# Kernel optimization log

Hardware: AMD Instinct MI355X
Metric: run time of the kernel (lower is better)

## Reference

```python
import jax, jax.numpy as jnp
import numpy as np

N_NODES = 50000
N_EDGES = 800000
IN_C, HID_C, OUT_C = 128, 128, 64


def setup_inputs() -> dict:
    key = jax.random.key(0)
    ks = jax.random.split(key, 12)
    glorot = lambda k, shape: jax.random.normal(k, shape, dtype=jnp.float32) * (2.0 / (shape[0] + shape[-1])) ** 0.5
    return {
        "x": jax.random.normal(ks[0], (N_NODES, IN_C), dtype=jnp.float32),
        "edge_index": jax.random.randint(ks[1], (2, N_EDGES), 0, N_NODES, dtype=jnp.int64),
        "W_s1": glorot(ks[2], (IN_C, HID_C)), "b_s1": jnp.zeros((HID_C,), jnp.float32),
        "W_s2": glorot(ks[3], (HID_C, HID_C)), "b_s2": jnp.zeros((HID_C,), jnp.float32),
        "W_m1": glorot(ks[4], (IN_C, HID_C)), "b_m1": jnp.zeros((HID_C,), jnp.float32),
        "W_m21": glorot(ks[5], (IN_C, HID_C)), "b_m21": jnp.zeros((HID_C,), jnp.float32),
        "W_m22": glorot(ks[6], (HID_C, HID_C)), "b_m22": jnp.zeros((HID_C,), jnp.float32),
        "W_att": glorot(ks[7], (HID_C, 1)), "b_att": jnp.zeros((1,), jnp.float32),
        "W_fc": glorot(ks[8], (2 * HID_C, OUT_C)), "b_fc": jnp.zeros((OUT_C,), jnp.float32),
    }


def _gcn_conv(x, W, b, src, dst, n_nodes):
    """PyG GCNConv: add self-loops, symmetric deg^-1/2 norm, linear, scatter-add, bias."""
    xw = x @ W  # [N, H]
    loop = jnp.arange(n_nodes, dtype=src.dtype)
    s = jnp.concatenate([src, loop])
    d = jnp.concatenate([dst, loop])
    ones = jnp.ones(s.shape[0], dtype=x.dtype)
    deg = jax.ops.segment_sum(ones, d, num_segments=n_nodes)  # in-degree incl. self loop
    dinv = jnp.where(deg > 0, jax.lax.rsqrt(deg), 0.0)
    norm = dinv[s] * dinv[d]  # [E+N]
    msg = xw[s] * norm[:, None]
    return jax.ops.segment_sum(msg, d, num_segments=n_nodes) + b


def reference(x, edge_index, W_s1, b_s1, W_s2, b_s2, W_m1, b_m1, W_m21, b_m21,
              W_m22, b_m22, W_att, b_att, W_fc, b_fc):
    n = x.shape[0]
    src, dst = edge_index[0], edge_index[1]
    # structural branch: two GCN layers
    h_struct = jax.nn.relu(_gcn_conv(x, W_s1, b_s1, src, dst, n))
    h_struct = jax.nn.relu(_gcn_conv(h_struct, W_s2, b_s2, src, dst, n))
    # meta branches
    h1 = jax.nn.relu(_gcn_conv(x, W_m1, b_m1, src, dst, n))
    h2 = jax.nn.relu(_gcn_conv(x, W_m21, b_m21, src, dst, n))
    h2 = jax.nn.relu(_gcn_conv(h2, W_m22, b_m22, src, dst, n))
    # attention-weighted fusion over the 2 branches
    H = jnp.stack([h1, h2], axis=1)  # [N, 2, H]
    attn_scores = H @ W_att + b_att  # [N, 2, 1]
    attn_weights = jax.nn.softmax(attn_scores, axis=1)
    h_meta = jnp.sum(attn_weights * H, axis=1)  # [N, H]
    h_comb = jnp.concatenate([h_struct, h_meta], axis=1)  # [N, 2H]
    return h_comb @ W_fc + b_fc  # [N, OUT_C]
```

## Files before the change

kernel.cpp:

```cpp
#include <hip/hip_runtime.h>
#include <hip/hip_bf16.h>

#define N_NODES 50000
#define N_EDGES 800000
#define IN_C 128
#define HID_C 128
#define OUT_C 64

#define SCAN_BS 256
#define SCAN_NB ((N_NODES + SCAN_BS - 1) / SCAN_BS)

#define PREP_CVT_NB   6250
#define PREP_DEG_NB   3125
#define PREP_WCAT_NB  192
#define PREP_TP_NB    64
#define PREP_NB (PREP_CVT_NB + PREP_DEG_NB + PREP_WCAT_NB + 3 * PREP_TP_NB)

typedef __attribute__((ext_vector_type(8))) short bf16x8;
typedef __attribute__((ext_vector_type(4))) float f32x4;

__device__ __forceinline__ ushort f2bf(float f) {
    unsigned u = __float_as_uint(f);
    return (ushort)((u + 0x7fffu + ((u >> 16) & 1u)) >> 16);
}
__device__ __forceinline__ float bf2f(ushort u) {
    return __uint_as_float(((unsigned)u) << 16);
}

__global__ __launch_bounds__(256)
void prep_kernel(const float* __restrict__ x, uint2* __restrict__ xb4,
                 const int* __restrict__ edst, int* __restrict__ hist,
                 const float* __restrict__ Ws1, const float* __restrict__ Wm21,
                 const float* __restrict__ Wm1,
                 const float* __restrict__ bs1, const float* __restrict__ bm21,
                 const float* __restrict__ bm1,
                 ushort* __restrict__ Wcat_t, float* __restrict__ bcat,
                 const float* __restrict__ Ws2, ushort* __restrict__ Ws2t,
                 const float* __restrict__ Wm22, ushort* __restrict__ Wm22t,
                 const float* __restrict__ Wfc, ushort* __restrict__ Wfct,
                 int* __restrict__ row_ptr) {
    const int bid = blockIdx.x;
    const int t = threadIdx.x;
    if (bid < PREP_CVT_NB) {
        int i = bid * 256 + t;
        float4 v = *(const float4*)&x[(size_t)i * 4];
        uint2 o;
        o.x = (uint)f2bf(v.x) | ((uint)f2bf(v.y) << 16);
        o.y = (uint)f2bf(v.z) | ((uint)f2bf(v.w) << 16);
        xb4[i] = o;
    } else if (bid < PREP_CVT_NB + PREP_DEG_NB) {
        int e = (bid - PREP_CVT_NB) * 256 + t;
        atomicAdd(&hist[edst[e]], 1);
    } else if (bid < PREP_CVT_NB + PREP_DEG_NB + PREP_WCAT_NB) {
        int idx = (bid - PREP_CVT_NB - PREP_DEG_NB) * 256 + t;
        int c = idx >> 7, k = idx & 127;
        float v = (c < 128) ? Ws1[k * 128 + c]
                : (c < 256) ? Wm21[k * 128 + (c - 128)]
                            : Wm1[k * 128 + (c - 256)];
        Wcat_t[idx] = f2bf(v);
        if (idx < 384) {
            bcat[idx] = (idx < 128) ? bs1[idx] : (idx < 256) ? bm21[idx - 128] : bm1[idx - 256];
        }
        if (idx == 0) row_ptr[N_NODES] = N_EDGES;
    } else if (bid < PREP_CVT_NB + PREP_DEG_NB + PREP_WCAT_NB + PREP_TP_NB) {
        int idx = (bid - PREP_CVT_NB - PREP_DEG_NB - PREP_WCAT_NB) * 256 + t;
        int c = idx >> 7, k = idx & 127;
        Ws2t[idx] = f2bf(Ws2[(size_t)k * 128 + c]);
    } else if (bid < PREP_CVT_NB + PREP_DEG_NB + PREP_WCAT_NB + 2 * PREP_TP_NB) {
        int idx = (bid - PREP_CVT_NB - PREP_DEG_NB - PREP_WCAT_NB - PREP_TP_NB) * 256 + t;
        int c = idx >> 7, k = idx & 127;
        Wm22t[idx] = f2bf(Wm22[(size_t)k * 128 + c]);
    } else {
        int idx = (bid - PREP_CVT_NB - PREP_DEG_NB - PREP_WCAT_NB - 2 * PREP_TP_NB) * 256 + t;
        int c = idx >> 8, k = idx & 255;
        Wfct[idx] = f2bf(Wfc[(size_t)k * 64 + c]);
    }
}

__global__ __launch_bounds__(SCAN_BS)
void scan1_kernel(const int* __restrict__ hist, int* __restrict__ bsum,
                  float* __restrict__ dinv, int n) {
    __shared__ int s[SCAN_BS];
    int t = threadIdx.x;
    int i = blockIdx.x * SCAN_BS + t;
    int v = (i < n) ? hist[i] : 0;
    if (i < n) dinv[i] = rsqrtf((float)(v + 1));
    s[t] = v;
    __syncthreads();
#pragma unroll
    for (int off = SCAN_BS / 2; off > 0; off >>= 1) {
        if (t < off) s[t] += s[t + off];
        __syncthreads();
    }
    if (t == 0) bsum[blockIdx.x] = s[0];
}

__global__ __launch_bounds__(SCAN_BS)
void scan3_kernel(const int* __restrict__ hist, const int* __restrict__ bsum,
                  int* __restrict__ row_ptr, int* __restrict__ cursor, int n) {
    __shared__ int s[SCAN_BS];
    __shared__ int pre_s;
    int t = threadIdx.x;
    int b = blockIdx.x;
    int p = 0;
    for (int j = t; j < b; j += SCAN_BS) p += bsum[j];
    s[t] = p;
    __syncthreads();
#pragma unroll
    for (int off = SCAN_BS / 2; off > 0; off >>= 1) {
        if (t < off) s[t] += s[t + off];
        __syncthreads();
    }
    if (t == 0) pre_s = s[0];
    __syncthreads();
    const int pre = pre_s;
    __syncthreads();
    int i = b * SCAN_BS + t;
    int v = (i < n) ? hist[i] : 0;
    s[t] = v;
    __syncthreads();
#pragma unroll
    for (int off = 1; off < SCAN_BS; off <<= 1) {
        int tmp = (t >= off) ? s[t - off] : 0;
        __syncthreads();
        s[t] += tmp;
        __syncthreads();
    }
    if (i < n) {
        int ex = s[t] - v + pre;
        row_ptr[i] = ex;
        cursor[i]  = ex;
    }
}

__global__ void fill_kernel(const int* __restrict__ src, const int* __restrict__ dst, int E,
                            int* __restrict__ cursor, int2* __restrict__ edge_data,
                            const float* __restrict__ dinv) {
    int e = blockIdx.x * blockDim.x + threadIdx.x;
    if (e < E) {
        int d = dst[e];
        int s = src[e];
        int pos = atomicAdd(&cursor[d], 1);
        edge_data[pos] = make_int2(s, __float_as_int(dinv[s]));
    }
}

template<int C>
__global__ __launch_bounds__(256)
void agg_bf16(const ushort* __restrict__ X, int ldx,
              ushort* __restrict__ Y, int ldy,
              const int* __restrict__ row_ptr,
              const int2* __restrict__ edge_data,
              const float* __restrict__ dinv, int n) {
    constexpr int CG = C / 8;
    constexpr int SLOTS = 64 / CG;
    const int wid = blockIdx.x * (blockDim.x >> 6) + (threadIdx.x >> 6);
    if (wid >= n) return;
    const int lane = threadIdx.x & 63;
    const int cg = lane & (CG - 1);
    const int slot = lane / CG;

    const float di = dinv[wid];
    float acc[8] = {0.f, 0.f, 0.f, 0.f, 0.f, 0.f, 0.f, 0.f};

    auto fma_row = [&](uint4 v, float w) {
        acc[0] = fmaf(w, __uint_as_float(v.x << 16), acc[0]);
        acc[1] = fmaf(w, __uint_as_float(v.x & 0xffff0000u), acc[1]);
        acc[2] = fmaf(w, __uint_as_float(v.y << 16), acc[2]);
        acc[3] = fmaf(w, __uint_as_float(v.y & 0xffff0000u), acc[3]);
        acc[4] = fmaf(w, __uint_as_float(v.z << 16), acc[4]);
        acc[5] = fmaf(w, __uint_as_float(v.z & 0xffff0000u), acc[5]);
        acc[6] = fmaf(w, __uint_as_float(v.w << 16), acc[6]);
        acc[7] = fmaf(w, __uint_as_float(v.w & 0xffff0000u), acc[7]);
    };

    if (slot == 0) {
        uint4 v = *(const uint4*)&X[(size_t)wid * ldx + cg * 8];
        fma_row(v, di * di);
    }
    const int e0 = row_ptr[wid], e1 = row_ptr[wid + 1];
    int e = e0 + slot;
    for (; e + 3 * SLOTS < e1; e += 4 * SLOTS) {
        const int2 d0 = edge_data[e];
        const int2 d1 = edge_data[e + SLOTS];
        const int2 d2 = edge_data[e + 2 * SLOTS];
        const int2 d3 = edge_data[e + 3 * SLOTS];
        const uint4 v0 = *(const uint4*)&X[(size_t)d0.x * ldx + cg * 8];
        const uint4 v1 = *(const uint4*)&X[(size_t)d1.x * ldx + cg * 8];
        const uint4 v2 = *(const uint4*)&X[(size_t)d2.x * ldx + cg * 8];
        const uint4 v3 = *(const uint4*)&X[(size_t)d3.x * ldx + cg * 8];
        fma_row(v0, di * __int_as_float(d0.y));
        fma_row(v1, di * __int_as_float(d1.y));
        fma_row(v2, di * __int_as_float(d2.y));
        fma_row(v3, di * __int_as_float(d3.y));
    }
    for (; e < e1; e += SLOTS) {
        const int2 d0 = edge_data[e];
        const uint4 v0 = *(const uint4*)&X[(size_t)d0.x * ldx + cg * 8];
        fma_row(v0, di * __int_as_float(d0.y));
    }
#pragma unroll
    for (int j = 0; j < 8; ++j) {
        if (SLOTS == 4) acc[j] += __shfl_xor(acc[j], 16);
        if (SLOTS >= 2) acc[j] += __shfl_xor(acc[j], 32);
    }
    if (slot == 0) {
        uint4 o;
        o.x = (uint)f2bf(acc[0]) | ((uint)f2bf(acc[1]) << 16);
        o.y = (uint)f2bf(acc[2]) | ((uint)f2bf(acc[3]) << 16);
        o.z = (uint)f2bf(acc[4]) | ((uint)f2bf(acc[5]) << 16);
        o.w = (uint)f2bf(acc[6]) | ((uint)f2bf(acc[7]) << 16);
        *(uint4*)&Y[(size_t)wid * ldy + cg * 8] = o;
    }
}

__global__ __launch_bounds__(256)
void mfma_gemm_kernel(const ushort* __restrict__ A, int lda,
                      const ushort* __restrict__ Wt,
                      const float* __restrict__ bias,
                      void* __restrict__ Yv, int ldy,
                      int M, int relu, int obf16) {
    __shared__ char Asmem[128 * 272];
    const int tid = threadIdx.x;
    const int lane = tid & 63;
    const int w = tid >> 6;
    const int rb = blockIdx.x * 128;
    const int cb = blockIdx.y * 128;

    {
        const int rowbase = tid >> 4;
        const int inrow = (tid & 15) * 8;
#pragma unroll
        for (int it = 0; it < 8; ++it) {
            int row = it * 16 + rowbase;
            uint4 v = make_uint4(0u, 0u, 0u, 0u);
            int r = rb + row;
            if (r < M) v = *(const uint4*)&A[(size_t)r * lda + inrow];
            *(uint4*)&Asmem[row * 272 + (tid & 15) * 16] = v;
        }
    }
    __syncthreads();

    f32x4 acc[2][8];
#pragma unroll
    for (int i = 0; i < 2; ++i)
#pragma unroll
        for (int j = 0; j < 8; ++j) acc[i][j] = (f32x4){0.f, 0.f, 0.f, 0.f};

    const int arow0 = w * 32 + (lane & 15);
    const int kq = (lane >> 4) * 8;
    const int ccol = lane & 15;
#pragma unroll
    for (int ks = 0; ks < 4; ++ks) {
        const int k0 = ks * 32;
        const bf16x8 a0 = *(const bf16x8*)&Asmem[arow0 * 272 + (k0 + kq) * 2];
        const bf16x8 a1 = *(const bf16x8*)&Asmem[(arow0 + 16) * 272 + (k0 + kq) * 2];
#pragma unroll
        for (int ct = 0; ct < 8; ++ct) {
            const bf16x8 b = *(const bf16x8*)&Wt[(size_t)(cb + ct * 16 + ccol) * 128 + k0 + kq];
            acc[0][ct] = __builtin_amdgcn_mfma_f32_16x16x32_bf16(a0, b, acc[0][ct], 0, 0, 0);
            acc[1][ct] = __builtin_amdgcn_mfma_f32_16x16x32_bf16(a1, b, acc[1][ct], 0, 0, 0);
        }
    }

    const int rowq = (lane >> 4) * 4;
#pragma unroll
    for (int rt = 0; rt < 2; ++rt) {
#pragma unroll
        for (int ct = 0; ct < 8; ++ct) {
            const int col = cb + ct * 16 + ccol;
            const float bcol = bias[col];
#pragma unroll
            for (int r = 0; r < 4; ++r) {
                const int row = rb + w * 32 + rt * 16 + rowq + r;
                if (row >= M) continue;
                float v = acc[rt][ct][r] + bcol;
                if (relu) v = fmaxf(v, 0.f);
                if (obf16) ((ushort*)Yv)[(size_t)row * ldy + col] = f2bf(v);
                else       ((float*)Yv)[(size_t)row * ldy + col] = v;
            }
        }
    }
}

__global__ __launch_bounds__(256)
void gemm2_kernel(const ushort* __restrict__ bufB,
                  const ushort* __restrict__ Ws2t, const float* __restrict__ bs2,
                  const ushort* __restrict__ Wm22t, const float* __restrict__ bm22,
                  const ushort* __restrict__ cat1,
                  const float* __restrict__ Watt, const float* __restrict__ batt,
                  ushort* __restrict__ comb, int M) {
    __shared__ char Asmem[128 * 272];
    const int tid = threadIdx.x;
    const int lane = tid & 63;
    const int w = tid >> 6;
    const int rb = blockIdx.x * 128;
    const int branch = blockIdx.y;
    const ushort* A = bufB + (branch ? 128 : 0);
    const ushort* Wt = branch ? Wm22t : Ws2t;
    const float* bias = branch ? bm22 : bs2;

    {
        const int rowbase = tid >> 4;
        const int seg = tid & 15;
#pragma unroll
        for (int it = 0; it < 8; ++it) {
            int row = it * 16 + rowbase;
            uint4 v = make_uint4(0u, 0u, 0u, 0u);
            int r = rb + row;
            if (r < M) v = *(const uint4*)&A[(size_t)r * 256 + seg * 8];
            *(uint4*)&Asmem[row * 272 + seg * 16] = v;
        }
    }
    __syncthreads();

    f32x4 acc[2][8];
#pragma unroll
    for (int i = 0; i < 2; ++i)
#pragma unroll
        for (int j = 0; j < 8; ++j) acc[i][j] = (f32x4){0.f, 0.f, 0.f, 0.f};

    const int arow0 = w * 32 + (lane & 15);
    const int kq = (lane >> 4) * 8;
    const int ccol = lane & 15;
#pragma unroll
    for (int ks = 0; ks < 4; ++ks) {
        const int k0 = ks * 32;
        const bf16x8 a0 = *(const bf16x8*)&Asmem[arow0 * 272 + (k0 + kq) * 2];
        const bf16x8 a1 = *(const bf16x8*)&Asmem[(arow0 + 16) * 272 + (k0 + kq) * 2];
#pragma unroll
        for (int ct = 0; ct < 8; ++ct) {
            const bf16x8 b = *(const bf16x8*)&Wt[(size_t)(ct * 16 + ccol) * 128 + k0 + kq];
            acc[0][ct] = __builtin_amdgcn_mfma_f32_16x16x32_bf16(a0, b, acc[0][ct], 0, 0, 0);
            acc[1][ct] = __builtin_amdgcn_mfma_f32_16x16x32_bf16(a1, b, acc[1][ct], 0, 0, 0);
        }
    }

    const int quad = lane >> 4;
    if (branch == 0) {
#pragma unroll
        for (int rt = 0; rt < 2; ++rt) {
#pragma unroll
            for (int ct = 0; ct < 8; ++ct) {
                const int col = ct * 16 + ccol;
                const float bcol = bias[col];
#pragma unroll
                for (int r = 0; r < 4; ++r) {
                    const int row = rb + w * 32 + rt * 16 + quad * 4 + r;
                    if (row >= M) continue;
                    comb[(size_t)row * 256 + col] = f2bf(fmaxf(acc[rt][ct][r] + bcol, 0.f));
                }
            }
        }
    } else {
#pragma unroll
        for (int rt = 0; rt < 2; ++rt)
#pragma unroll
            for (int ct = 0; ct < 8; ++ct) {
                const float bcol = bias[ct * 16 + ccol];
#pragma unroll
                for (int r = 0; r < 4; ++r)
                    acc[rt][ct][r] = fmaxf(acc[rt][ct][r] + bcol, 0.f);
            }
        float wv[8];
#pragma unroll
        for (int ct = 0; ct < 8; ++ct) wv[ct] = Watt[ct * 16 + ccol];
        const float ba = batt[0];
#pragma unroll
        for (int rt = 0; rt < 2; ++rt) {
#pragma unroll
            for (int r = 0; r < 4; ++r) {
                const int row0 = rb + w * 32 + rt * 16 + quad * 4 + r;
                const int rowc = (row0 < M) ? row0 : (M - 1);
                const ushort* h1row = &cat1[(size_t)rowc * 384 + 256];
                float bp = 0.f, ap = 0.f;
#pragma unroll
                for (int ct = 0; ct < 8; ++ct) {
                    bp += acc[rt][ct][r] * wv[ct];
                    ap += bf2f(h1row[ct * 16 + ccol]) * wv[ct];
                }
#pragma unroll
                for (int off = 1; off < 16; off <<= 1) {
                    bp += __shfl_xor(bp, off);
                    ap += __shfl_xor(ap, off);
                }
                const float a = ap + ba, b = bp + ba;
                const float m = fmaxf(a, b);
                const float ea = __expf(a - m), eb = __expf(b - m);
                const float inv = 1.f / (ea + eb);
                const float wa = ea * inv, wb = eb * inv;
                if (row0 < M) {
#pragma unroll
                    for (int ct = 0; ct < 8; ++ct) {
                        const float h1 = bf2f(h1row[ct * 16 + ccol]);
                        comb[(size_t)row0 * 256 + 128 + ct * 16 + ccol] =
                            f2bf(fmaf(wa, h1, wb * acc[rt][ct][r]));
                    }
                }
            }
        }
    }
}

__global__ __launch_bounds__(256)
void mfma_fc_kernel(const ushort* __restrict__ A,
                    const ushort* __restrict__ Wt,
                    const float* __restrict__ bias,
                    float* __restrict__ Y, int M) {
    __shared__ char Asmem[64 * 528];
    const int tid = threadIdx.x;
    const int lane = tid & 63;
    const int w = tid >> 6;
    const int rb = blockIdx.x * 64;

    {
        const int rowbase = tid >> 5;
        const int seg = (tid & 31);
#pragma unroll
        for (int it = 0; it < 8; ++it) {
            int row = it * 8 + rowbase;
            uint4 v = make_uint4(0u, 0u, 0u, 0u);
            int r = rb + row;
            if (r < M) v = *(const uint4*)&A[(size_t)r * 256 + seg * 8];
            *(uint4*)&Asmem[row * 528 + seg * 16] = v;
        }
    }
    __syncthreads();

    f32x4 acc[4];
#pragma unroll
    for (int j = 0; j < 4; ++j) acc[j] = (f32x4){0.f, 0.f, 0.f, 0.f};

    const int arow = w * 16 + (lane & 15);
    const int kq = (lane >> 4) * 8;
    const int ccol = lane & 15;
#pragma unroll
    for (int ks = 0; ks < 8; ++ks) {
        const int k0 = ks * 32;
        const bf16x8 a = *(const bf16x8*)&Asmem[arow * 528 + (k0 + kq) * 2];
#pragma unroll
        for (int ct = 0; ct < 4; ++ct) {
            const bf16x8 b = *(const bf16x8*)&Wt[(size_t)(ct * 16 + ccol) * 256 + k0 + kq];
            acc[ct] = __builtin_amdgcn_mfma_f32_16x16x32_bf16(a, b, acc[ct], 0, 0, 0);
        }
    }

    const int rowq = (lane >> 4) * 4;
#pragma unroll
    for (int ct = 0; ct < 4; ++ct) {
        const int col = ct * 16 + ccol;
        const float bcol = bias[col];
#pragma unroll
        for (int r = 0; r < 4; ++r) {
            const int row = rb + w * 16 + rowq + r;
            if (row < M) Y[(size_t)row * 64 + col] = acc[ct][r] + bcol;
        }
    }
}

extern "C" void kernel_launch(void* const* d_in, const int* in_sizes, int n_in,
                              void* d_out, int out_size, void* d_ws, size_t ws_size,
                              hipStream_t stream) {
    const int N = N_NODES, E = N_EDGES;
    const float* x     = (const float*)d_in[0];
    const int*   ei    = (const int*)d_in[1];
    const int*   esrc  = ei;
    const int*   edst  = ei + E;
    const float* W_s1  = (const float*)d_in[2];
    const float* b_s1  = (const float*)d_in[3];
    const float* W_s2  = (const float*)d_in[4];
    const float* b_s2  = (const float*)d_in[5];
    const float* W_m1  = (const float*)d_in[6];
    const float* b_m1  = (const float*)d_in[7];
    const float* W_m21 = (const float*)d_in[8];
    const float* b_m21 = (const float*)d_in[9];
    const float* W_m22 = (const float*)d_in[10];
    const float* b_m22 = (const float*)d_in[11];
    const float* W_att = (const float*)d_in[12];
    const float* b_att = (const float*)d_in[13];
    const float* W_fc  = (const float*)d_in[14];
    const float* b_fc  = (const float*)d_in[15];
    float* out = (float*)d_out;

    char* base = (char*)d_ws;
    size_t off = 0;
    auto take = [&](size_t nbytes) -> void* {
        void* p = base + off;
        off += (nbytes + 255) & ~(size_t)255;
        return p;
    };
    int*    hist      = (int*)take((size_t)N * 4);
    int*    cursor    = (int*)take((size_t)N * 4);
    int*    row_ptr   = (int*)take((size_t)(N + 1) * 4);
    int*    bsum      = (int*)take((size_t)SCAN_NB * 4);
    int2*   edge_data = (int2*)take((size_t)E * 8);
    float*  dinv      = (float*)take((size_t)N * 4);
    ushort* xb        = (ushort*)take((size_t)N * 128 * 2);
    ushort* agg_x     = (ushort*)take((size_t)N * 128 * 2);
    ushort* cat1      = (ushort*)take((size_t)N * 384 * 2);
    ushort* bufB      = (ushort*)take((size_t)N * 256 * 2);
    ushort* comb      = (ushort*)take((size_t)N * 256 * 2);
    ushort* Wcat_t    = (ushort*)take((size_t)384 * 128 * 2);
    ushort* Ws2_t     = (ushort*)take((size_t)128 * 128 * 2);
    ushort* Wm22_t    = (ushort*)take((size_t)128 * 128 * 2);
    ushort* Wfc_t     = (ushort*)take((size_t)64 * 256 * 2);
    float*  bcat      = (float*)take((size_t)384 * 4);

    hipMemsetAsync(hist, 0, (size_t)N * 4, stream);
    prep_kernel<<<PREP_NB, 256, 0, stream>>>(x, (uint2*)xb, edst, hist,
                                             W_s1, W_m21, W_m1, b_s1, b_m21, b_m1,
                                             Wcat_t, bcat, W_s2, Ws2_t, W_m22, Wm22_t,
                                             W_fc, Wfc_t, row_ptr);
    scan1_kernel<<<SCAN_NB, SCAN_BS, 0, stream>>>(hist, bsum, dinv, N);
    scan3_kernel<<<SCAN_NB, SCAN_BS, 0, stream>>>(hist, bsum, row_ptr, cursor, N);
    fill_kernel<<<(E + 255) / 256, 256, 0, stream>>>(esrc, edst, E, cursor, edge_data, dinv);

    agg_bf16<128><<<(N + 3) / 4, 256, 0, stream>>>(xb, 128, agg_x, 128, row_ptr, edge_data, dinv, N);
    dim3 gm384((N + 127) / 128, 3);
    mfma_gemm_kernel<<<gm384, 256, 0, stream>>>(agg_x, 128, Wcat_t, bcat, cat1, 384, N, 1, 1);
    agg_bf16<256><<<(N + 3) / 4, 256, 0, stream>>>(cat1, 384, bufB, 256, row_ptr, edge_data, dinv, N);
    dim3 gm2((N + 127) / 128, 2);
    gemm2_kernel<<<gm2, 256, 0, stream>>>(bufB, Ws2_t, b_s2, Wm22_t, b_m22,
                                          cat1, W_att, b_att, comb, N);
    mfma_fc_kernel<<<(N + 63) / 64, 256, 0, stream>>>(comb, Wfc_t, b_fc, out, N);
}
```

Baseline: 383.6 us.

## Fuse all pipeline stages into one persistent cooperative kernel with grid syncs

Replaces the sequence of separate kernels (prep, scans, CSR fill, two aggregations, three GEMMs) with a single cooperatively launched persistent kernel. Grid-wide barriers separate the stages and work is distributed with grid-stride loops. The aim is to remove per-launch overhead and the idle gaps between kernels. The cost is grid.sync overhead at each stage, occupancy capped by the largest stage's register and shared-memory needs, and less parallelism in the small stages.

```diff
diff --git a/kernel.cpp b/kernel.cpp
--- a/kernel.cpp
+++ b/kernel.cpp
@@ -1,20 +1,13 @@
 #include <hip/hip_runtime.h>
 #include <hip/hip_bf16.h>
+#include <hip/hip_cooperative_groups.h>
+
+namespace cg = cooperative_groups;
 
 #define N_NODES 50000
 #define N_EDGES 800000
-#define IN_C 128
-#define HID_C 128
-#define OUT_C 64
-
 #define SCAN_BS 256
 #define SCAN_NB ((N_NODES + SCAN_BS - 1) / SCAN_BS)
-
-#define PREP_CVT_NB   6250
-#define PREP_DEG_NB   3125
-#define PREP_WCAT_NB  192
-#define PREP_TP_NB    64
-#define PREP_NB (PREP_CVT_NB + PREP_DEG_NB + PREP_WCAT_NB + 3 * PREP_TP_NB)
 
 typedef __attribute__((ext_vector_type(8))) short bf16x8;
 typedef __attribute__((ext_vector_type(4))) float f32x4;
@@ -27,139 +20,31 @@
     return __uint_as_float(((unsigned)u) << 16);
 }
 
-__global__ __launch_bounds__(256)
-void prep_kernel(const float* __restrict__ x, uint2* __restrict__ xb4,
-                 const int* __restrict__ edst, int* __restrict__ hist,
-                 const float* __restrict__ Ws1, const float* __restrict__ Wm21,
-                 const float* __restrict__ Wm1,
-                 const float* __restrict__ bs1, const float* __restrict__ bm21,
-                 const float* __restrict__ bm1,
-                 ushort* __restrict__ Wcat_t, float* __restrict__ bcat,
-                 const float* __restrict__ Ws2, ushort* __restrict__ Ws2t,
-                 const float* __restrict__ Wm22, ushort* __restrict__ Wm22t,
-                 const float* __restrict__ Wfc, ushort* __restrict__ Wfct,
-                 int* __restrict__ row_ptr) {
-    const int bid = blockIdx.x;
-    const int t = threadIdx.x;
-    if (bid < PREP_CVT_NB) {
-        int i = bid * 256 + t;
-        float4 v = *(const float4*)&x[(size_t)i * 4];
-        uint2 o;
-        o.x = (uint)f2bf(v.x) | ((uint)f2bf(v.y) << 16);
-        o.y = (uint)f2bf(v.z) | ((uint)f2bf(v.w) << 16);
-        xb4[i] = o;
-    } else if (bid < PREP_CVT_NB + PREP_DEG_NB) {
-        int e = (bid - PREP_CVT_NB) * 256 + t;
-        atomicAdd(&hist[edst[e]], 1);
-    } else if (bid < PREP_CVT_NB + PREP_DEG_NB + PREP_WCAT_NB) {
-        int idx = (bid - PREP_CVT_NB - PREP_DEG_NB) * 256 + t;
-        int c = idx >> 7, k = idx & 127;
-        float v = (c < 128) ? Ws1[k * 128 + c]
-                : (c < 256) ? Wm21[k * 128 + (c - 128)]
-                            : Wm1[k * 128 + (c - 256)];
-        Wcat_t[idx] = f2bf(v);
-        if (idx < 384) {
-            bcat[idx] = (idx < 128) ? bs1[idx] : (idx < 256) ? bm21[idx - 128] : bm1[idx - 256];
-        }
-        if (idx == 0) row_ptr[N_NODES] = N_EDGES;
-    } else if (bid < PREP_CVT_NB + PREP_DEG_NB + PREP_WCAT_NB + PREP_TP_NB) {
-        int idx = (bid - PREP_CVT_NB - PREP_DEG_NB - PREP_WCAT_NB) * 256 + t;
-        int c = idx >> 7, k = idx & 127;
-        Ws2t[idx] = f2bf(Ws2[(size_t)k * 128 + c]);
-    } else if (bid < PREP_CVT_NB + PREP_DEG_NB + PREP_WCAT_NB + 2 * PREP_TP_NB) {
-        int idx = (bid - PREP_CVT_NB - PREP_DEG_NB - PREP_WCAT_NB - PREP_TP_NB) * 256 + t;
-        int c = idx >> 7, k = idx & 127;
-        Wm22t[idx] = f2bf(Wm22[(size_t)k * 128 + c]);
-    } else {
-        int idx = (bid - PREP_CVT_NB - PREP_DEG_NB - PREP_WCAT_NB - 2 * PREP_TP_NB) * 256 + t;
-        int c = idx >> 8, k = idx & 255;
-        Wfct[idx] = f2bf(Wfc[(size_t)k * 64 + c]);
-    }
-}
-
-__global__ __launch_bounds__(SCAN_BS)
-void scan1_kernel(const int* __restrict__ hist, int* __restrict__ bsum,
-                  float* __restrict__ dinv, int n) {
-    __shared__ int s[SCAN_BS];
-    int t = threadIdx.x;
-    int i = blockIdx.x * SCAN_BS + t;
-    int v = (i < n) ? hist[i] : 0;
-    if (i < n) dinv[i] = rsqrtf((float)(v + 1));
-    s[t] = v;
-    __syncthreads();
-#pragma unroll
-    for (int off = SCAN_BS / 2; off > 0; off >>= 1) {
-        if (t < off) s[t] += s[t + off];
-        __syncthreads();
-    }
-    if (t == 0) bsum[blockIdx.x] = s[0];
-}
-
-__global__ __launch_bounds__(SCAN_BS)
-void scan3_kernel(const int* __restrict__ hist, const int* __restrict__ bsum,
-                  int* __restrict__ row_ptr, int* __restrict__ cursor, int n) {
-    __shared__ int s[SCAN_BS];
-    __shared__ int pre_s;
-    int t = threadIdx.x;
-    int b = blockIdx.x;
-    int p = 0;
-    for (int j = t; j < b; j += SCAN_BS) p += bsum[j];
-    s[t] = p;
-    __syncthreads();
-#pragma unroll
-    for (int off = SCAN_BS / 2; off > 0; off >>= 1) {
-        if (t < off) s[t] += s[t + off];
-        __syncthreads();
-    }
-    if (t == 0) pre_s = s[0];
-    __syncthreads();
-    const int pre = pre_s;
-    __syncthreads();
-    int i = b * SCAN_BS + t;
-    int v = (i < n) ? hist[i] : 0;
-    s[t] = v;
-    __syncthreads();
-#pragma unroll
-    for (int off = 1; off < SCAN_BS; off <<= 1) {
-        int tmp = (t >= off) ? s[t - off] : 0;
-        __syncthreads();
-        s[t] += tmp;
-        __syncthreads();
-    }
-    if (i < n) {
-        int ex = s[t] - v + pre;
-        row_ptr[i] = ex;
-        cursor[i]  = ex;
-    }
-}
-
-__global__ void fill_kernel(const int* __restrict__ src, const int* __restrict__ dst, int E,
-                            int* __restrict__ cursor, int2* __restrict__ edge_data,
-                            const float* __restrict__ dinv) {
-    int e = blockIdx.x * blockDim.x + threadIdx.x;
-    if (e < E) {
-        int d = dst[e];
-        int s = src[e];
-        int pos = atomicAdd(&cursor[d], 1);
-        edge_data[pos] = make_int2(s, __float_as_int(dinv[s]));
-    }
-}
+struct MegaParams {
+    const float* x;
+    const int* esrc;
+    const int* edst;
+    const float *Ws1, *bs1, *Ws2, *bs2, *Wm1, *bm1, *Wm21, *bm21, *Wm22, *bm22;
+    const float *Watt, *batt, *Wfc, *bfc;
+    float* out;
+    int* hist; int* cursor; int* row_ptr; int* bsum;
+    int2* edge_data; float* dinv;
+    ushort *xb, *agg_x, *cat1, *bufB, *comb;
+    ushort *Wcat_t, *Ws2t, *Wm22t, *Wfct;
+    float* bcat;
+};
 
 template<int C>
-__global__ __launch_bounds__(256)
-void agg_bf16(const ushort* __restrict__ X, int ldx,
-              ushort* __restrict__ Y, int ldy,
-              const int* __restrict__ row_ptr,
-              const int2* __restrict__ edge_data,
-              const float* __restrict__ dinv, int n) {
+__device__ __forceinline__ void agg_node(const ushort* __restrict__ X, int ldx,
+                                         ushort* __restrict__ Y, int ldy,
+                                         const int* __restrict__ row_ptr,
+                                         const int2* __restrict__ edge_data,
+                                         const float* __restrict__ dinv,
+                                         int wid, int lane) {
     constexpr int CG = C / 8;
     constexpr int SLOTS = 64 / CG;
-    const int wid = blockIdx.x * (blockDim.x >> 6) + (threadIdx.x >> 6);
-    if (wid >= n) return;
-    const int lane = threadIdx.x & 63;
-    const int cg = lane & (CG - 1);
+    const int cgi = lane & (CG - 1);
     const int slot = lane / CG;
-
     const float di = dinv[wid];
     float acc[8] = {0.f, 0.f, 0.f, 0.f, 0.f, 0.f, 0.f, 0.f};
 
@@ -175,7 +60,7 @@
     };
 
     if (slot == 0) {
-        uint4 v = *(const uint4*)&X[(size_t)wid * ldx + cg * 8];
+        uint4 v = *(const uint4*)&X[(size_t)wid * ldx + cgi * 8];
         fma_row(v, di * di);
     }
     const int e0 = row_ptr[wid], e1 = row_ptr[wid + 1];
@@ -185,10 +70,10 @@
         const int2 d1 = edge_data[e + SLOTS];
         const int2 d2 = edge_data[e + 2 * SLOTS];
         const int2 d3 = edge_data[e + 3 * SLOTS];
-        const uint4 v0 = *(const uint4*)&X[(size_t)d0.x * ldx + cg * 8];
-        const uint4 v1 = *(const uint4*)&X[(size_t)d1.x * ldx + cg * 8];
-        const uint4 v2 = *(const uint4*)&X[(size_t)d2.x * ldx + cg * 8];
-        const uint4 v3 = *(const uint4*)&X[(size_t)d3.x * ldx + cg * 8];
+        const uint4 v0 = *(const uint4*)&X[(size_t)d0.x * ldx + cgi * 8];
+        const uint4 v1 = *(const uint4*)&X[(size_t)d1.x * ldx + cgi * 8];
+        const uint4 v2 = *(const uint4*)&X[(size_t)d2.x * ldx + cgi * 8];
+        const uint4 v3 = *(const uint4*)&X[(size_t)d3.x * ldx + cgi * 8];
         fma_row(v0, di * __int_as_float(d0.y));
         fma_row(v1, di * __int_as_float(d1.y));
         fma_row(v2, di * __int_as_float(d2.y));
@@ -196,7 +81,7 @@
     }
     for (; e < e1; e += SLOTS) {
         const int2 d0 = edge_data[e];
-        const uint4 v0 = *(const uint4*)&X[(size_t)d0.x * ldx + cg * 8];
+        const uint4 v0 = *(const uint4*)&X[(size_t)d0.x * ldx + cgi * 8];
         fma_row(v0, di * __int_as_float(d0.y));
     }
 #pragma unroll
@@ -210,33 +95,26 @@
         o.y = (uint)f2bf(acc[2]) | ((uint)f2bf(acc[3]) << 16);
         o.z = (uint)f2bf(acc[4]) | ((uint)f2bf(acc[5]) << 16);
         o.w = (uint)f2bf(acc[6]) | ((uint)f2bf(acc[7]) << 16);
-        *(uint4*)&Y[(size_t)wid * ldy + cg * 8] = o;
-    }
-}
-
-__global__ __launch_bounds__(256)
-void mfma_gemm_kernel(const ushort* __restrict__ A, int lda,
-                      const ushort* __restrict__ Wt,
-                      const float* __restrict__ bias,
-                      void* __restrict__ Yv, int ldy,
-                      int M, int relu, int obf16) {
-    __shared__ char Asmem[128 * 272];
-    const int tid = threadIdx.x;
+        *(uint4*)&Y[(size_t)wid * ldy + cgi * 8] = o;
+    }
+}
+
+__device__ __forceinline__ void gemm128_tile(char* smem,
+        const ushort* __restrict__ A, int lda,
+        const ushort* __restrict__ Wt, const float* __restrict__ bias,
+        ushort* __restrict__ Y, int ldy, int rb, int cb, int M, int tid) {
     const int lane = tid & 63;
     const int w = tid >> 6;
-    const int rb = blockIdx.x * 128;
-    const int cb = blockIdx.y * 128;
-
     {
         const int rowbase = tid >> 4;
-        const int inrow = (tid & 15) * 8;
+        const int seg = tid & 15;
 #pragma unroll
         for (int it = 0; it < 8; ++it) {
             int row = it * 16 + rowbase;
             uint4 v = make_uint4(0u, 0u, 0u, 0u);
             int r = rb + row;
-            if (r < M) v = *(const uint4*)&A[(size_t)r * lda + inrow];
-            *(uint4*)&Asmem[row * 272 + (tid & 15) * 16] = v;
+            if (r < M) v = *(const uint4*)&A[(size_t)r * lda + seg * 8];
+            *(uint4*)&smem[row * 272 + seg * 16] = v;
         }
     }
     __syncthreads();
@@ -253,8 +131,8 @@
 #pragma unroll
     for (int ks = 0; ks < 4; ++ks) {
         const int k0 = ks * 32;
-        const bf16x8 a0 = *(const bf16x8*)&Asmem[arow0 * 272 + (k0 + kq) * 2];
-        const bf16x8 a1 = *(const bf16x8*)&Asmem[(arow0 + 16) * 272 + (k0 + kq) * 2];
+        const bf16x8 a0 = *(const bf16x8*)&smem[arow0 * 272 + (k0 + kq) * 2];
+        const bf16x8 a1 = *(const bf16x8*)&smem[(arow0 + 16) * 272 + (k0 + kq) * 2];
 #pragma unroll
         for (int ct = 0; ct < 8; ++ct) {
             const bf16x8 b = *(const bf16x8*)&Wt[(size_t)(cb + ct * 16 + ccol) * 128 + k0 + kq];
@@ -274,31 +152,21 @@
             for (int r = 0; r < 4; ++r) {
                 const int row = rb + w * 32 + rt * 16 + rowq + r;
                 if (row >= M) continue;
-                float v = acc[rt][ct][r] + bcol;
-                if (relu) v = fmaxf(v, 0.f);
-                if (obf16) ((ushort*)Yv)[(size_t)row * ldy + col] = f2bf(v);
-                else       ((float*)Yv)[(size_t)row * ldy + col] = v;
+                Y[(size_t)row * ldy + col] = f2bf(fmaxf(acc[rt][ct][r] + bcol, 0.f));
             }
         }
     }
-}
-
-__global__ __launch_bounds__(256)
-void gemm2_kernel(const ushort* __restrict__ bufB,
-                  const ushort* __restrict__ Ws2t, const float* __restrict__ bs2,
-                  const ushort* __restrict__ Wm22t, const float* __restrict__ bm22,
-                  const ushort* __restrict__ cat1,
-                  const float* __restrict__ Watt, const float* __restrict__ batt,
-                  ushort* __restrict__ comb, int M) {
-    __shared__ char Asmem[128 * 272];
-    const int tid = threadIdx.x;
+    __syncthreads();
+}
+
+__device__ __forceinline__ void gemm2_tile(char* smem, const MegaParams& p,
+                                           int rb, int branch, int tid) {
     const int lane = tid & 63;
     const int w = tid >> 6;
-    const int rb = blockIdx.x * 128;
-    const int branch = blockIdx.y;
-    const ushort* A = bufB + (branch ? 128 : 0);
-    const ushort* Wt = branch ? Wm22t : Ws2t;
-    const float* bias = branch ? bm22 : bs2;
+    const int M = N_NODES;
+    const ushort* A = p.bufB + (branch ? 128 : 0);
+    const ushort* Wt = branch ? p.Wm22t : p.Ws2t;
+    const float* bias = branch ? p.bm22 : p.bs2;
 
     {
         const int rowbase = tid >> 4;
@@ -309,7 +177,7 @@
             uint4 v = make_uint4(0u, 0u, 0u, 0u);
             int r = rb + row;
             if (r < M) v = *(const uint4*)&A[(size_t)r * 256 + seg * 8];
-            *(uint4*)&Asmem[row * 272 + seg * 16] = v;
+            *(uint4*)&smem[row * 272 + seg * 16] = v;
         }
     }
     __syncthreads();
@@ -326,8 +194,8 @@
 #pragma unroll
     for (int ks = 0; ks < 4; ++ks) {
         const int k0 = ks * 32;
-        const bf16x8 a0 = *(const bf16x8*)&Asmem[arow0 * 272 + (k0 + kq) * 2];
-        const bf16x8 a1 = *(const bf16x8*)&Asmem[(arow0 + 16) * 272 + (k0 + kq) * 2];
+        const bf16x8 a0 = *(const bf16x8*)&smem[arow0 * 272 + (k0 + kq) * 2];
+        const bf16x8 a1 = *(const bf16x8*)&smem[(arow0 + 16) * 272 + (k0 + kq) * 2];
 #pragma unroll
         for (int ct = 0; ct < 8; ++ct) {
             const bf16x8 b = *(const bf16x8*)&Wt[(size_t)(ct * 16 + ccol) * 128 + k0 + kq];
@@ -348,7 +216,7 @@
                 for (int r = 0; r < 4; ++r) {
                     const int row = rb + w * 32 + rt * 16 + quad * 4 + r;
                     if (row >= M) continue;
-                    comb[(size_t)row * 256 + col] = f2bf(fmaxf(acc[rt][ct][r] + bcol, 0.f));
+                    p.comb[(size_t)row * 256 + col] = f2bf(fmaxf(acc[rt][ct][r] + bcol, 0.f));
                 }
             }
         }
@@ -364,15 +232,15 @@
             }
         float wv[8];
 #pragma unroll
-        for (int ct = 0; ct < 8; ++ct) wv[ct] = Watt[ct * 16 + ccol];
-        const float ba = batt[0];
+        for (int ct = 0; ct < 8; ++ct) wv[ct] = p.Watt[ct * 16 + ccol];
+        const float ba = p.batt[0];
 #pragma unroll
         for (int rt = 0; rt < 2; ++rt) {
 #pragma unroll
             for (int r = 0; r < 4; ++r) {
                 const int row0 = rb + w * 32 + rt * 16 + quad * 4 + r;
                 const int rowc = (row0 < M) ? row0 : (M - 1);
-                const ushort* h1row = &cat1[(size_t)rowc * 384 + 256];
+                const ushort* h1row = &p.cat1[(size_t)rowc * 384 + 256];
                 float bp = 0.f, ap = 0.f;
 #pragma unroll
                 for (int ct = 0; ct < 8; ++ct) {
@@ -393,36 +261,32 @@
 #pragma unroll
                     for (int ct = 0; ct < 8; ++ct) {
                         const float h1 = bf2f(h1row[ct * 16 + ccol]);
-                        comb[(size_t)row0 * 256 + 128 + ct * 16 + ccol] =
+                        p.comb[(size_t)row0 * 256 + 128 + ct * 16 + ccol] =
                             f2bf(fmaf(wa, h1, wb * acc[rt][ct][r]));
                     }
                 }
             }
         }
     }
-}
-
-__global__ __launch_bounds__(256)
-void mfma_fc_kernel(const ushort* __restrict__ A,
-                    const ushort* __restrict__ Wt,
-                    const float* __restrict__ bias,
-                    float* __restrict__ Y, int M) {
-    __shared__ char Asmem[64 * 528];
-    const int tid = threadIdx.x;
+    __syncthreads();
+}
+
+__device__ __forceinline__ void fc_tile(char* smem,
+        const ushort* __restrict__ A, const ushort* __restrict__ Wt,
+        const float* __restrict__ bias, float* __restrict__ Y,
+        int rb, int M, int tid) {
     const int lane = tid & 63;
     const int w = tid >> 6;
-    const int rb = blockIdx.x * 64;
-
     {
         const int rowbase = tid >> 5;
-        const int seg = (tid & 31);
+        const int seg = tid & 31;
 #pragma unroll
         for (int it = 0; it < 8; ++it) {
             int row = it * 8 + rowbase;
             uint4 v = make_uint4(0u, 0u, 0u, 0u);
             int r = rb + row;
             if (r < M) v = *(const uint4*)&A[(size_t)r * 256 + seg * 8];
-            *(uint4*)&Asmem[row * 528 + seg * 16] = v;
+            *(uint4*)&smem[row * 528 + seg * 16] = v;
         }
     }
     __syncthreads();
@@ -437,7 +301,7 @@
 #pragma unroll
     for (int ks = 0; ks < 8; ++ks) {
         const int k0 = ks * 32;
-        const bf16x8 a = *(const bf16x8*)&Asmem[arow * 528 + (k0 + kq) * 2];
+        const bf16x8 a = *(const bf16x8*)&smem[arow * 528 + (k0 + kq) * 2];
 #pragma unroll
         for (int ct = 0; ct < 4; ++ct) {
             const bf16x8 b = *(const bf16x8*)&Wt[(size_t)(ct * 16 + ccol) * 256 + k0 + kq];
@@ -455,6 +319,150 @@
             const int row = rb + w * 16 + rowq + r;
             if (row < M) Y[(size_t)row * 64 + col] = acc[ct][r] + bcol;
         }
+    }
+    __syncthreads();
+}
+
+__global__ __launch_bounds__(256, 4)
+void mega_kernel(MegaParams p) {
+    cg::grid_group grid = cg::this_grid();
+    const int tid = threadIdx.x;
+    const int gtid = blockIdx.x * 256 + tid;
+    const int T = gridDim.x * 256;
+    const int lane = tid & 63;
+    const int gw = gtid >> 6;
+    const int WG = T >> 6;
+
+    __shared__ __align__(16) char smem[128 * 272];
+    __shared__ int pre_s;
+
+    for (int i = gtid; i < N_NODES; i += T) p.hist[i] = 0;
+    {
+        uint2* xb4 = (uint2*)p.xb;
+        const int n4 = N_NODES * 128 / 4;
+        for (int i = gtid; i < n4; i += T) {
+            float4 v = *(const float4*)&p.x[(size_t)i * 4];
+            uint2 o;
+            o.x = (uint)f2bf(v.x) | ((uint)f2bf(v.y) << 16);
+            o.y = (uint)f2bf(v.z) | ((uint)f2bf(v.w) << 16);
+            xb4[i] = o;
+        }
+    }
+    for (int idx = gtid; idx < 384 * 128; idx += T) {
+        int c = idx >> 7, k = idx & 127;
+        float v = (c < 128) ? p.Ws1[k * 128 + c]
+                : (c < 256) ? p.Wm21[k * 128 + (c - 128)]
+                            : p.Wm1[k * 128 + (c - 256)];
+        p.Wcat_t[idx] = f2bf(v);
+        if (idx < 384)
+            p.bcat[idx] = (idx < 128) ? p.bs1[idx] : (idx < 256) ? p.bm21[idx - 128] : p.bm1[idx - 256];
+        if (idx == 0) p.row_ptr[N_NODES] = N_EDGES;
+    }
+    for (int idx = gtid; idx < 128 * 128; idx += T) {
+        int c = idx >> 7, k = idx & 127;
+        p.Ws2t[idx]  = f2bf(p.Ws2[(size_t)k * 128 + c]);
+        p.Wm22t[idx] = f2bf(p.Wm22[(size_t)k * 128 + c]);
+    }
+    for (int idx = gtid; idx < 64 * 256; idx += T) {
+        int c = idx >> 8, k = idx & 255;
+        p.Wfct[idx] = f2bf(p.Wfc[(size_t)k * 64 + c]);
+    }
+    grid.sync();
+
+    for (int e = gtid; e < N_EDGES; e += T) atomicAdd(&p.hist[p.edst[e]], 1);
+    grid.sync();
+
+    for (int b = blockIdx.x; b < SCAN_NB; b += gridDim.x) {
+        int* s = (int*)smem;
+        int i = b * SCAN_BS + tid;
+        int v = (i < N_NODES) ? p.hist[i] : 0;
+        if (i < N_NODES) p.dinv[i] = rsqrtf((float)(v + 1));
+        s[tid] = v;
+        __syncthreads();
+#pragma unroll
+        for (int off = SCAN_BS / 2; off > 0; off >>= 1) {
+            if (tid < off) s[tid] += s[tid + off];
+            __syncthreads();
+        }
+        if (tid == 0) p.bsum[b] = s[0];
+        __syncthreads();
+    }
+    grid.sync();
+
+    for (int b = blockIdx.x; b < SCAN_NB; b += gridDim.x) {
+        int* s = (int*)smem;
+        int pv = 0;
+        for (int j = tid; j < b; j += SCAN_BS) pv += p.bsum[j];
+        s[tid] = pv;
+        __syncthreads();
+#pragma unroll
+        for (int off = SCAN_BS / 2; off > 0; off >>= 1) {
+            if (tid < off) s[tid] += s[tid + off];
+            __syncthreads();
+        }
+        if (tid == 0) pre_s = s[0];
+        __syncthreads();
+        const int pre = pre_s;
+        __syncthreads();
+        int i = b * SCAN_BS + tid;
+        int v = (i < N_NODES) ? p.hist[i] : 0;
+        s[tid] = v;
+        __syncthreads();
+#pragma unroll
+        for (int off = 1; off < SCAN_BS; off <<= 1) {
+            int tmp = (tid >= off) ? s[tid - off] : 0;
+            __syncthreads();
+            s[tid] += tmp;
+            __syncthreads();
+        }
+        if (i < N_NODES) {
+            int ex = s[tid] - v + pre;
+            p.row_ptr[i] = ex;
+            p.cursor[i]  = ex;
+        }
+        __syncthreads();
+    }
+    grid.sync();
+
+    for (int e = gtid; e < N_EDGES; e += T) {
+        int d = p.edst[e];
+        int sI = p.esrc[e];
+        int pos = atomicAdd(&p.cursor[d], 1);
+        p.edge_data[pos] = make_int2(sI, __float_as_int(p.dinv[sI]));
+    }
+    grid.sync();
+
+    for (int node = gw; node < N_NODES; node += WG)
+        agg_node<128>(p.xb, 128, p.agg_x, 128, p.row_ptr, p.edge_data, p.dinv, node, lane);
+    grid.sync();
+
+    {
+        const int RT = (N_NODES + 127) / 128;
+        for (int t = blockIdx.x; t < RT * 3; t += gridDim.x) {
+            int rbi = t % RT, cbi = t / RT;
+            gemm128_tile(smem, p.agg_x, 128, p.Wcat_t, p.bcat, p.cat1, 384,
+                         rbi * 128, cbi * 128, N_NODES, tid);
+        }
+    }
+    grid.sync();
+
+    for (int node = gw; node < N_NODES; node += WG)
+        agg_node<256>(p.cat1, 384, p.bufB, 256, p.row_ptr, p.edge_data, p.dinv, node, lane);
+    grid.sync();
+
+    {
+        const int RT = (N_NODES + 127) / 128;
+        for (int t = blockIdx.x; t < RT * 2; t += gridDim.x) {
+            int rbi = t % RT, branch = t / RT;
+            gemm2_tile(smem, p, rbi * 128, branch, tid);
+        }
+    }
+    grid.sync();
+
+    {
+        const int RT = (N_NODES + 63) / 64;
+        for (int t = blockIdx.x; t < RT; t += gridDim.x)
+            fc_tile(smem, p.comb, p.Wfct, p.bfc, p.out, t * 64, N_NODES, tid);
     }
 }
 
@@ -462,65 +470,52 @@
                               void* d_out, int out_size, void* d_ws, size_t ws_size,
                               hipStream_t stream) {
     const int N = N_NODES, E = N_EDGES;
-    const float* x     = (const float*)d_in[0];
-    const int*   ei    = (const int*)d_in[1];
-    const int*   esrc  = ei;
-    const int*   edst  = ei + E;
-    const float* W_s1  = (const float*)d_in[2];
-    const float* b_s1  = (const float*)d_in[3];
-    const float* W_s2  = (const float*)d_in[4];
-    const float* b_s2  = (const float*)d_in[5];
-    const float* W_m1  = (const float*)d_in[6];
-    const float* b_m1  = (const float*)d_in[7];
-    const float* W_m21 = (const float*)d_in[8];
-    const float* b_m21 = (const float*)d_in[9];
-    const float* W_m22 = (const float*)d_in[10];
-    const float* b_m22 = (const float*)d_in[11];
-    const float* W_att = (const float*)d_in[12];
-    const float* b_att = (const float*)d_in[13];
-    const float* W_fc  = (const float*)d_in[14];
-    const float* b_fc  = (const float*)d_in[15];
-    float* out = (float*)d_out;
+
+    MegaParams p;
+    p.x    = (const float*)d_in[0];
+    const int* ei = (const int*)d_in[1];
+    p.esrc = ei;
+    p.edst = ei + E;
+    p.Ws1  = (const float*)d_in[2];  p.bs1  = (const float*)d_in[3];
+    p.Ws2  = (const float*)d_in[4];  p.bs2  = (const float*)d_in[5];
+    p.Wm1  = (const float*)d_in[6];  p.bm1  = (const float*)d_in[7];
+    p.Wm21 = (const float*)d_in[8];  p.bm21 = (const float*)d_in[9];
+    p.Wm22 = (const float*)d_in[10]; p.bm22 = (const float*)d_in[11];
+    p.Watt = (const float*)d_in[12]; p.batt = (const float*)d_in[13];
+    p.Wfc  = (const float*)d_in[14]; p.bfc  = (const float*)d_in[15];
+    p.out  = (float*)d_out;
 
     char* base = (char*)d_ws;
     size_t off = 0;
     auto take = [&](size_t nbytes) -> void* {
-        void* p = base + off;
+        void* ptr = base + off;
         off += (nbytes + 255) & ~(size_t)255;
-        return p;
+        return ptr;
     };
-    int*    hist      = (int*)take((size_t)N * 4);
-    int*    cursor    = (int*)take((size_t)N * 4);
-    int*    row_ptr   = (int*)take((size_t)(N + 1) * 4);
-    int*    bsum      = (int*)take((size_t)SCAN_NB * 4);
-    int2*   edge_data = (int2*)take((size_t)E * 8);
-    float*  dinv      = (float*)take((size_t)N * 4);
-    ushort* xb        = (ushort*)take((size_t)N * 128 * 2);
-    ushort* agg_x     = (ushort*)take((size_t)N * 128 * 2);
-    ushort* cat1      = (ushort*)take((size_t)N * 384 * 2);
-    ushort* bufB      = (ushort*)take((size_t)N * 256 * 2);
-    ushort* comb      = (ushort*)take((size_t)N * 256 * 2);
-    ushort* Wcat_t    = (ushort*)take((size_t)384 * 128 * 2);
-    ushort* Ws2_t     = (ushort*)take((size_t)128 * 128 * 2);
-    ushort* Wm22_t    = (ushort*)take((size_t)128 * 128 * 2);
-    ushort* Wfc_t     = (ushort*)take((size_t)64 * 256 * 2);
-    float*  bcat      = (float*)take((size_t)384 * 4);
-
-    hipMemsetAsync(hist, 0, (size_t)N * 4, stream);
-    prep_kernel<<<PREP_NB, 256, 0, stream>>>(x, (uint2*)xb, edst, hist,
-                                             W_s1, W_m21, W_m1, b_s1, b_m21, b_m1,
-                                             Wcat_t, bcat, W_s2, Ws2_t, W_m22, Wm22_t,
-                                             W_fc, Wfc_t, row_ptr);
-    scan1_kernel<<<SCAN_NB, SCAN_BS, 0, stream>>>(hist, bsum, dinv, N);
-    scan3_kernel<<<SCAN_NB, SCAN_BS, 0, stream>>>(hist, bsum, row_ptr, cursor, N);
-    fill_kernel<<<(E + 255) / 256, 256, 0, stream>>>(esrc, edst, E, cursor, edge_data, dinv);
-
-    agg_bf16<128><<<(N + 3) / 4, 256, 0, stream>>>(xb, 128, agg_x, 128, row_ptr, edge_data, dinv, N);
-    dim3 gm384((N + 127) / 128, 3);
-    mfma_gemm_kernel<<<gm384, 256, 0, stream>>>(agg_x, 128, Wcat_t, bcat, cat1, 384, N, 1, 1);
-    agg_bf16<256><<<(N + 3) / 4, 256, 0, stream>>>(cat1, 384, bufB, 256, row_ptr, edge_data, dinv, N);
-    dim3 gm2((N + 127) / 128, 2);
-    gemm2_kernel<<<gm2, 256, 0, stream>>>(bufB, Ws2_t, b_s2, Wm22_t, b_m22,
-                                          cat1, W_att, b_att, comb, N);
-    mfma_fc_kernel<<<(N + 63) / 64, 256, 0, stream>>>(comb, Wfc_t, b_fc, out, N);
-}
+    p.hist      = (int*)take((size_t)N * 4);
+    p.cursor    = (int*)take((size_t)N * 4);
+    p.row_ptr   = (int*)take((size_t)(N + 1) * 4);
+    p.bsum      = (int*)take((size_t)SCAN_NB * 4);
+    p.edge_data = (int2*)take((size_t)E * 8);
+    p.dinv      = (float*)take((size_t)N * 4);
+    p.xb        = (ushort*)take((size_t)N * 128 * 2);
+    p.agg_x     = (ushort*)take((size_t)N * 128 * 2);
+    p.cat1      = (ushort*)take((size_t)N * 384 * 2);
+    p.bufB      = (ushort*)take((size_t)N * 256 * 2);
+    p.comb      = (ushort*)take((size_t)N * 256 * 2);
+    p.Wcat_t    = (ushort*)take((size_t)384 * 128 * 2);
+    p.Ws2t      = (ushort*)take((size_t)128 * 128 * 2);
+    p.Wm22t     = (ushort*)take((size_t)128 * 128 * 2);
+    p.Wfct      = (ushort*)take((size_t)64 * 256 * 2);
+    p.bcat      = (float*)take((size_t)384 * 4);
+
+    int maxb = 0;
+    hipOccupancyMaxActiveBlocksPerMultiprocessor(&maxb, mega_kernel, 256, 0);
+    if (maxb < 1) maxb = 1;
+    if (maxb > 8) maxb = 8;
+    int grid = 256 * maxb;
+    if (grid > 2048) grid = 2048;
+
+    void* kargs[] = { (void*)&p };
+    hipLaunchCooperativeKernel(mega_kernel, dim3(grid), dim3(256), kargs, 0, stream);
+}
```

After: 1.015 ms. +164.6%, slower.
